# Kernel optimization log

Hardware: AMD Instinct MI355X
Metric: run time of the kernel (lower is better)

## Reference

```python
import jax, jax.numpy as jnp
import numpy as np

P_SCALAR = 40.0
NEG_INF = -1e30


def setup_inputs() -> dict:
    key = jax.random.key(0)
    k1, k2, k3, k4, k5 = jax.random.split(key, 5)
    B, Dk, Dv, T, H, W = 8, 128, 512, 2, 56, 56
    qkey = jax.random.normal(k1, (B, Dk, H, W), dtype=jnp.float32)
    qmask = jax.random.randint(k2, (B, 1, H, W), 0, 2).astype(jnp.bool_)
    mkey = jax.random.normal(k3, (B, Dk, T, H, W), dtype=jnp.float32)
    mval = jax.random.normal(k4, (B, Dv, T, H, W), dtype=jnp.float32)
    mmask = jax.random.randint(k5, (B, 1, T, H, W), 0, 2).astype(jnp.bool_)
    return {"qkey": qkey, "qmask": qmask, "mkey": mkey, "mval": mval, "mmask": mmask}


def reference(qkey, qmask, mkey, mval, mmask):
    # Faithful vectorized version of SegmentationAttentionSeparateModule.maskRead.
    # Torch loops over b, gathers masked query/memory columns, does
    # softmax(p_scalar * mk^T qk, dim=0) then mv @ p, scattering into zeros.
    # Equivalent dense math: masked softmax over memory positions, and zero
    # output at query positions outside qmask.
    B, Dk, H, W = qkey.shape
    Dv = mval.shape[1]
    M = H * W                       # query positions
    qk = qkey.reshape(B, Dk, M)     # [B, Dk, M]
    mk = mkey.reshape(B, Dk, -1)    # [B, Dk, N], N = T*H*W
    mv = mval.reshape(B, Dv, -1)    # [B, Dv, N]
    qm = qmask.reshape(B, 1, M)     # [B, 1, M]
    mm = mmask.reshape(B, -1)       # [B, N]

    # scores over memory (axis 1) per query column, p_scalar * mk^T qk
    scores = P_SCALAR * jnp.einsum('bdn,bdm->bnm', mk, qk)       # [B, N, M]
    scores = jnp.where(mm[:, :, None], scores, NEG_INF)
    p = jax.nn.softmax(scores, axis=1)                           # softmax over memory
    p = jnp.where(mm[:, :, None], p, 0.0)                        # guard all-masked rows
    qread = jnp.einsum('bdn,bnm->bdm', mv, p)                    # [B, Dv, M]
    qread = jnp.where(qm, qread, 0.0)                            # only masked query cols
    return qread.reshape(B, Dv, H, W)
```

## Files before the change

### kernel.cpp

```cpp
#include <hip/hip_runtime.h>
#include <stdint.h>

#define B_    8
#define DK_   128
#define DV_   512
#define M_    3136
#define N_    6272
#define MTILES_ 49
#define NSEG_ 8
#define TH_   30.0f
#define MARGIN_ 36.0f
#define BKT_  64

typedef short bf16x8 __attribute__((ext_vector_type(8)));
typedef float f32x16 __attribute__((ext_vector_type(16)));
typedef unsigned short u16x8 __attribute__((ext_vector_type(8)));

__device__ __forceinline__ unsigned fkey(float x) {
  unsigned u = __float_as_uint(x);
  return (u & 0x80000000u) ? ~u : (u | 0x80000000u);
}
__device__ __forceinline__ float fdec(unsigned k) {
  return __uint_as_float((k & 0x80000000u) ? (k & 0x7fffffffu) : ~k);
}
__device__ __forceinline__ unsigned short f2bf(float x) {
  unsigned u = __float_as_uint(x);
  return (unsigned short)((u + 0x7fffu + ((u >> 16) & 1u)) >> 16);
}
__device__ __forceinline__ unsigned pk2(float x, float y) {
  return (unsigned)f2bf(x) | ((unsigned)f2bf(y) << 16);
}
__device__ __forceinline__ float bf2f(unsigned short h) {
  return __uint_as_float(((unsigned)h) << 16);
}

__global__ __launch_bounds__(256)
void scan_masks(const int* __restrict__ qmask, const int* __restrict__ mmask,
                int* __restrict__ qlist, int* __restrict__ nlist,
                int* __restrict__ qcnt, int* __restrict__ ncnt) {
  int b = blockIdx.x;
  int tid = threadIdx.x, lane = tid & 63, wv = tid >> 6;
  __shared__ int wsum[4];
  __shared__ int cbase;
  if (tid == 0) cbase = 0;
  __syncthreads();
  for (int base = 0; base < M_; base += 256) {
    int i = base + tid;
    int flag = (i < M_) ? (qmask[b * M_ + i] != 0) : 0;
    unsigned long long bal = __ballot(flag);
    int prefix = __popcll(bal & ((1ull << lane) - 1ull));
    if (lane == 0) wsum[wv] = __popcll(bal);
    __syncthreads();
    int woff = 0;
    for (int t = 0; t < wv; ++t) woff += wsum[t];
    int total = wsum[0] + wsum[1] + wsum[2] + wsum[3];
    if (flag) qlist[b * M_ + cbase + woff + prefix] = i;
    __syncthreads();
    if (tid == 0) cbase += total;
    __syncthreads();
  }
  if (tid == 0) { qcnt[b] = cbase; cbase = 0; }
  __syncthreads();
  for (int base = 0; base < N_; base += 256) {
    int i = base + tid;
    int flag = (i < N_) ? (mmask[b * N_ + i] != 0) : 0;
    unsigned long long bal = __ballot(flag);
    int prefix = __popcll(bal & ((1ull << lane) - 1ull));
    if (lane == 0) wsum[wv] = __popcll(bal);
    __syncthreads();
    int woff = 0;
    for (int t = 0; t < wv; ++t) woff += wsum[t];
    int total = wsum[0] + wsum[1] + wsum[2] + wsum[3];
    if (flag) nlist[b * N_ + cbase + woff + prefix] = i;
    __syncthreads();
    if (tid == 0) cbase += total;
    __syncthreads();
  }
  if (tid == 0) ncnt[b] = cbase;
}

__global__ __launch_bounds__(256)
void transpose_key(const float* __restrict__ src, float* __restrict__ dst,
                   int X, float scale) {
  __shared__ float T[64][65];
  int b = blockIdx.z, dt = blockIdx.y, xt = blockIdx.x;
  int lane = threadIdx.x & 63, ri = threadIdx.x >> 6;
  #pragma unroll
  for (int k = 0; k < 16; ++k) {
    int dl = ri * 16 + k;
    T[dl][lane] = src[((size_t)b * DK_ + dt * 64 + dl) * X + xt * 64 + lane];
  }
  __syncthreads();
  #pragma unroll
  for (int k = 0; k < 16; ++k) {
    int xl = ri * 16 + k;
    dst[((size_t)b * X + xt * 64 + xl) * DK_ + dt * 64 + lane] = scale * T[lane][xl];
  }
}

__global__ __launch_bounds__(256)
void transpose_val(const float* __restrict__ mval, unsigned short* __restrict__ mvalT) {
  __shared__ float T[64][65];
  int b = blockIdx.z, dvt = blockIdx.y, nt = blockIdx.x;
  int lane = threadIdx.x & 63, ri = threadIdx.x >> 6;
  #pragma unroll
  for (int k = 0; k < 16; ++k) {
    int dvl = ri * 16 + k;
    T[dvl][lane] = mval[((size_t)b * DV_ + dvt * 64 + dvl) * N_ + nt * 64 + lane];
  }
  __syncthreads();
  #pragma unroll
  for (int k = 0; k < 16; ++k) {
    int nl = ri * 16 + k;
    mvalT[((size_t)b * N_ + nt * 64 + nl) * DV_ + dvt * 64 + lane] = f2bf(T[lane][nl]);
  }
}

__global__ __launch_bounds__(256, 4)
void score_mfma(const float* __restrict__ qkeyT, const float* __restrict__ mkeyT,
                const int* __restrict__ qlist, const int* __restrict__ nlist,
                const int* __restrict__ qcnt, const int* __restrict__ ncnt,
                unsigned* __restrict__ maxkey, unsigned* __restrict__ bcnt,
                unsigned* __restrict__ bucket) {
  int bid = blockIdx.x;
  int seg = bid & (NSEG_ - 1);
  int t   = bid >> 3;
  int mt  = t % MTILES_;
  int b   = t / MTILES_;
  int mc = qcnt[b];
  if (mt * 64 >= mc) return;
  int nc = ncnt[b];
  int ntiles = (nc + 63) >> 6;
  int t0 = (ntiles * seg) / NSEG_;
  int t1 = (ntiles * (seg + 1)) / NSEG_;
  if (t0 >= t1) return;

  __shared__ unsigned short Qs[64 * 128];
  __shared__ unsigned short Ks[64 * 128];
  __shared__ int Morig[64];
  __shared__ int Norig[64];
  __shared__ unsigned runkey[64];
  char* Qsb = (char*)Qs;
  char* Ksb = (char*)Ks;

  int tid = threadIdx.x;
  int lane = tid & 63, wv = tid >> 6;
  int wn = wv & 1, wm = wv >> 1;
  int l31 = lane & 31, lhi = lane >> 5;

  for (int i = tid; i < 2048; i += 256) {
    int row = i >> 5;
    int k4 = (i & 31) << 2;
    int cm = mt * 64 + row;
    int col = (cm < mc) ? qlist[b * M_ + cm] : qlist[b * M_];
    if (k4 == 0) Morig[row] = (cm < mc) ? col : -1;
    float4 v = *(const float4*)&qkeyT[((size_t)b * M_ + col) * DK_ + k4];
    uint2 w;
    w.x = pk2(v.x, v.y);
    w.y = pk2(v.z, v.w);
    *(uint2*)(Qsb + (row << 8) + (((unsigned)(k4 << 1)) ^ ((row & 7) << 4))) = w;
  }
  if (tid < 64) runkey[tid] = 0u;
  __syncthreads();

  int arow = wn * 32 + l31;
  int brow = wm * 32 + l31;
  int klo  = lhi << 4;
  int aswz = (arow & 7) << 4;
  int bswz = (brow & 7) << 4;

  for (int tt = t0; tt < t1; ++tt) {
    int nbase = tt << 6;
    for (int i = tid; i < 2048; i += 256) {
      int row = i >> 5;
      int k4 = (i & 31) << 2;
      int jn = nbase + row;
      int ncol = (jn < nc) ? nlist[b * N_ + jn] : nlist[b * N_];
      if (k4 == 0) Norig[row] = (jn < nc) ? ncol : -1;
      float4 v = *(const float4*)&mkeyT[((size_t)b * N_ + ncol) * DK_ + k4];
      uint2 w;
      w.x = pk2(v.x, v.y);
      w.y = pk2(v.z, v.w);
      *(uint2*)(Ksb + (row << 8) + (((unsigned)(k4 << 1)) ^ ((row & 7) << 4))) = w;
    }
    __syncthreads();

    f32x16 acc;
    #pragma unroll
    for (int r = 0; r < 16; ++r) acc[r] = 0.0f;
    #pragma unroll
    for (int kc = 0; kc < 8; ++kc) {
      int koff = (kc << 5) | klo;
      bf16x8 af = *(const bf16x8*)(Ksb + (arow << 8) + (koff ^ aswz));
      bf16x8 bq = *(const bf16x8*)(Qsb + (brow << 8) + (koff ^ bswz));
      acc = __builtin_amdgcn_mfma_f32_32x32x16_bf16(af, bq, acc, 0, 0, 0);
    }

    float cmx = acc[0];
    #pragma unroll
    for (int r = 1; r < 16; ++r) cmx = fmaxf(cmx, acc[r]);
    cmx = fmaxf(cmx, __shfl_xor(cmx, 32));
    if (lane < 32) atomicMax(&runkey[wm * 32 + l31], fkey(cmx));
    __syncthreads();
    if (tid < 64 && Morig[tid] >= 0) {
      unsigned mine = runkey[tid];
      unsigned old = atomicMax(&maxkey[b * M_ + Morig[tid]], mine);
      if (old > mine) runkey[tid] = old;
    }
    __syncthreads();
    {
      int mloc = wm * 32 + l31;
      int mo = Morig[mloc];
      if (mo >= 0) {
        float thr = fdec(runkey[mloc]) - MARGIN_;
        #pragma unroll
        for (int r = 0; r < 16; ++r) {
          if (acc[r] >= thr) {
            int nl = wn * 32 + (r & 3) + ((r >> 2) << 3) + (lhi << 2);
            int no = Norig[nl];
            if (no >= 0) {
              unsigned slot = atomicAdd(&bcnt[b * M_ + mo], 1u);
              if (slot < (unsigned)BKT_)
                bucket[(((size_t)(b * M_ + mo)) << 6) + slot] = (unsigned)no;
            }
          }
        }
      }
    }
    __syncthreads();
  }
}

__device__ __forceinline__ float dot128(const float* __restrict__ q,
                                        const float* __restrict__ k) {
  float s = 0.f;
  #pragma unroll 8
  for (int i = 0; i < DK_; i += 4) {
    float4 a = *(const float4*)&q[i];
    float4 bb = *(const float4*)&k[i];
    s += a.x * bb.x + a.y * bb.y + a.z * bb.z + a.w * bb.w;
  }
  return s;
}

__global__ __launch_bounds__(256)
void pv_exact(const float* __restrict__ qkeyT, const float* __restrict__ mkeyT,
              const unsigned short* __restrict__ mvalT,
              const int* __restrict__ qlist, const int* __restrict__ qcnt,
              const int* __restrict__ nlist, const int* __restrict__ ncnt,
              const unsigned* __restrict__ bcnt, const unsigned* __restrict__ bucket,
              float* __restrict__ outT) {
  int b = blockIdx.y;
  int wv = threadIdx.x >> 6, lane = threadIdx.x & 63;
  int c = blockIdx.x * 4 + wv;
  if (c >= qcnt[b]) return;
  int m = qlist[b * M_ + c];
  unsigned cnt = bcnt[b * M_ + m];
  const float* qrow = qkeyT + ((size_t)b * M_ + m) * DK_;
  float acc[8] = {0.f, 0.f, 0.f, 0.f, 0.f, 0.f, 0.f, 0.f};
  float lsum = 0.f;

  if (cnt <= (unsigned)BKT_) {
    int n = -1;
    if (lane < (int)cnt) n = (int)bucket[(((size_t)(b * M_ + m)) << 6) + lane];
    float sv = -3.0e38f;
    if (n >= 0) sv = dot128(qrow, mkeyT + ((size_t)b * N_ + n) * DK_);
    float mx = sv;
    #pragma unroll
    for (int o = 32; o > 0; o >>= 1) mx = fmaxf(mx, __shfl_xor(mx, o));
    float e = (n >= 0 && sv >= mx - TH_) ? expf(sv - mx) : 0.f;
    lsum = e;
    #pragma unroll
    for (int o = 32; o > 0; o >>= 1) lsum += __shfl_xor(lsum, o);
    unsigned long long alive = __ballot(e > 0.f);
    while (alive) {
      int lb = __ffsll((unsigned long long)alive) - 1;
      alive &= alive - 1;
      float w = __shfl(e, lb);
      int nn = __shfl(n, lb);
      u16x8 vvv = *(const u16x8*)(mvalT + ((size_t)b * N_ + nn) * DV_ + lane * 8);
      #pragma unroll
      for (int r = 0; r < 8; ++r) acc[r] += w * bf2f(vvv[r]);
    }
  } else {
    int nc = ncnt[b];
    float mx = -3.0e38f;
    for (int base = 0; base < nc; base += 64) {
      int jn = base + lane;
      float sv = -3.0e38f;
      if (jn < nc) {
        int n = nlist[b * N_ + jn];
        sv = dot128(qrow, mkeyT + ((size_t)b * N_ + n) * DK_);
      }
      mx = fmaxf(mx, sv);
    }
    #pragma unroll
    for (int o = 32; o > 0; o >>= 1) mx = fmaxf(mx, __shfl_xor(mx, o));
    for (int base = 0; base < nc; base += 64) {
      int jn = base + lane;
      int n = -1;
      float sv = -3.0e38f;
      if (jn < nc) {
        n = nlist[b * N_ + jn];
        sv = dot128(qrow, mkeyT + ((size_t)b * N_ + n) * DK_);
      }
      float e = (n >= 0 && sv >= mx - TH_) ? expf(sv - mx) : 0.f;
      lsum += e;
      unsigned long long alive = __ballot(e > 0.f);
      while (alive) {
        int lb = __ffsll((unsigned long long)alive) - 1;
        alive &= alive - 1;
        float w = __shfl(e, lb);
        int nn = __shfl(n, lb);
        u16x8 vvv = *(const u16x8*)(mvalT + ((size_t)b * N_ + nn) * DV_ + lane * 8);
        #pragma unroll
        for (int r = 0; r < 8; ++r) acc[r] += w * bf2f(vvv[r]);
      }
    }
    #pragma unroll
    for (int o = 32; o > 0; o >>= 1) lsum += __shfl_xor(lsum, o);
  }

  float inv = (lsum > 0.f) ? 1.0f / lsum : 0.0f;
  float* op = outT + ((size_t)b * M_ + m) * DV_ + lane * 8;
  float4 o0 = make_float4(acc[0] * inv, acc[1] * inv, acc[2] * inv, acc[3] * inv);
  float4 o1 = make_float4(acc[4] * inv, acc[5] * inv, acc[6] * inv, acc[7] * inv);
  *(float4*)&op[0] = o0;
  *(float4*)&op[4] = o1;
}

__global__ __launch_bounds__(256)
void finalize_T(const float* __restrict__ outT, const int* __restrict__ qmask,
                float* __restrict__ out) {
  __shared__ float T[64][65];
  int b = blockIdx.z, dvt = blockIdx.y, mt = blockIdx.x;
  int lane = threadIdx.x & 63, ri = threadIdx.x >> 6;
  #pragma unroll
  for (int k = 0; k < 16; ++k) {
    int ml = ri * 16 + k;
    int m = mt * 64 + ml;
    bool act = (qmask[b * M_ + m] != 0);
    T[ml][lane] = act ? outT[((size_t)b * M_ + m) * DV_ + dvt * 64 + lane] : 0.f;
  }
  __syncthreads();
  #pragma unroll
  for (int k = 0; k < 16; ++k) {
    int dvl = ri * 16 + k;
    out[((size_t)b * DV_ + dvt * 64 + dvl) * M_ + mt * 64 + lane] = T[lane][dvl];
  }
}

extern "C" void kernel_launch(void* const* d_in, const int* in_sizes, int n_in,
                              void* d_out, int out_size, void* d_ws, size_t ws_size,
                              hipStream_t stream) {
  const float* qkey  = (const float*)d_in[0];
  const int*   qmask = (const int*)d_in[1];
  const float* mkey  = (const float*)d_in[2];
  const float* mval  = (const float*)d_in[3];
  const int*   mmask = (const int*)d_in[4];
  float* out = (float*)d_out;

  uint8_t* w = (uint8_t*)d_ws;
  unsigned*       maxkey = (unsigned*)(w + 0);
  unsigned*       bcnt   = (unsigned*)(w + 100352);
  int*            qcnt   = (int*)(w + 200704);
  int*            ncnt   = (int*)(w + 200736);
  int*            qlist  = (int*)(w + 200832);
  int*            nlist  = (int*)(w + 301184);
  unsigned*       bucket = (unsigned*)(w + 501888);
  float*          qkeyT  = (float*)(w + 6924416);
  float*          mkeyT  = (float*)(w + 19769472);
  float*          outT   = (float*)(w + 45459584);
  unsigned short* mvalT  = (unsigned short*)(w + 96839808);

  hipMemsetAsync(d_ws, 0, 200832, stream);

  scan_masks<<<B_, 256, 0, stream>>>(qmask, mmask, qlist, nlist, qcnt, ncnt);
  transpose_key<<<dim3(M_ / 64, DK_ / 64, B_), 256, 0, stream>>>(qkey, qkeyT, M_, 40.0f);
  transpose_key<<<dim3(N_ / 64, DK_ / 64, B_), 256, 0, stream>>>(mkey, mkeyT, N_, 1.0f);
  transpose_val<<<dim3(N_ / 64, DV_ / 64, B_), 256, 0, stream>>>(mval, mvalT);

  score_mfma<<<B_ * MTILES_ * NSEG_, 256, 0, stream>>>(
      qkeyT, mkeyT, qlist, nlist, qcnt, ncnt, maxkey, bcnt, bucket);

  pv_exact<<<dim3((M_ + 3) / 4, B_), 256, 0, stream>>>(
      qkeyT, mkeyT, mvalT, qlist, qcnt, nlist, ncnt, bcnt, bucket, outT);

  finalize_T<<<dim3(M_ / 64, DV_ / 64, B_), 256, 0, stream>>>(outT, qmask, out);
}
```

Measured before the change: 229.6 us.

## Enlarge score tiles, precompute bf16 keys, bf16 output staging, parallel mask scans

The score kernel now covers 128 query rows per block, with each wave computing two 32x32 MFMA tiles that share one query fragment, and it loads bf16 keys prepared ahead of time by the transpose kernels. The per-tile float-to-bf16 packing is gone. Mask scans for query and memory run in separate blocks. The intermediate output is stored as bf16 rather than fp32, roughly halving its traffic but lowering its precision before finalize. The transposes now write both fp32 and bf16 copies, and the larger LDS footprint reduces occupancy.

```diff
diff --git a/kernel.cpp b/kernel.cpp
--- a/kernel.cpp
+++ b/kernel.cpp
@@ -6,7 +6,7 @@
 #define DV_   512
 #define M_    3136
 #define N_    6272
-#define MTILES_ 49
+#define MT128_ 25
 #define NSEG_ 8
 #define TH_   30.0f
 #define MARGIN_ 36.0f
@@ -26,9 +26,6 @@
 __device__ __forceinline__ unsigned short f2bf(float x) {
   unsigned u = __float_as_uint(x);
   return (unsigned short)((u + 0x7fffu + ((u >> 16) & 1u)) >> 16);
-}
-__device__ __forceinline__ unsigned pk2(float x, float y) {
-  return (unsigned)f2bf(x) | ((unsigned)f2bf(y) << 16);
 }
 __device__ __forceinline__ float bf2f(unsigned short h) {
   return __uint_as_float(((unsigned)h) << 16);
@@ -44,9 +41,12 @@
   __shared__ int cbase;
   if (tid == 0) cbase = 0;
   __syncthreads();
-  for (int base = 0; base < M_; base += 256) {
+  const int* src = (blockIdx.y == 0) ? (qmask + b * M_) : (mmask + b * N_);
+  int* dst = (blockIdx.y == 0) ? (qlist + b * M_) : (nlist + b * N_);
+  int len = (blockIdx.y == 0) ? M_ : N_;
+  for (int base = 0; base < len; base += 256) {
     int i = base + tid;
-    int flag = (i < M_) ? (qmask[b * M_ + i] != 0) : 0;
+    int flag = (i < len) ? (src[i] != 0) : 0;
     unsigned long long bal = __ballot(flag);
     int prefix = __popcll(bal & ((1ull << lane) - 1ull));
     if (lane == 0) wsum[wv] = __popcll(bal);
@@ -54,34 +54,19 @@
     int woff = 0;
     for (int t = 0; t < wv; ++t) woff += wsum[t];
     int total = wsum[0] + wsum[1] + wsum[2] + wsum[3];
-    if (flag) qlist[b * M_ + cbase + woff + prefix] = i;
+    if (flag) dst[cbase + woff + prefix] = i;
     __syncthreads();
     if (tid == 0) cbase += total;
     __syncthreads();
   }
-  if (tid == 0) { qcnt[b] = cbase; cbase = 0; }
-  __syncthreads();
-  for (int base = 0; base < N_; base += 256) {
-    int i = base + tid;
-    int flag = (i < N_) ? (mmask[b * N_ + i] != 0) : 0;
-    unsigned long long bal = __ballot(flag);
-    int prefix = __popcll(bal & ((1ull << lane) - 1ull));
-    if (lane == 0) wsum[wv] = __popcll(bal);
-    __syncthreads();
-    int woff = 0;
-    for (int t = 0; t < wv; ++t) woff += wsum[t];
-    int total = wsum[0] + wsum[1] + wsum[2] + wsum[3];
-    if (flag) nlist[b * N_ + cbase + woff + prefix] = i;
-    __syncthreads();
-    if (tid == 0) cbase += total;
-    __syncthreads();
-  }
-  if (tid == 0) ncnt[b] = cbase;
-}
-
-__global__ __launch_bounds__(256)
-void transpose_key(const float* __restrict__ src, float* __restrict__ dst,
-                   int X, float scale) {
+  if (tid == 0) {
+    if (blockIdx.y == 0) qcnt[b] = cbase; else ncnt[b] = cbase;
+  }
+}
+
+__global__ __launch_bounds__(256)
+void transpose_key(const float* __restrict__ src, float* __restrict__ dstf,
+                   unsigned short* __restrict__ dstb, int X, float scale) {
   __shared__ float T[64][65];
   int b = blockIdx.z, dt = blockIdx.y, xt = blockIdx.x;
   int lane = threadIdx.x & 63, ri = threadIdx.x >> 6;
@@ -94,7 +79,10 @@
   #pragma unroll
   for (int k = 0; k < 16; ++k) {
     int xl = ri * 16 + k;
-    dst[((size_t)b * X + xt * 64 + xl) * DK_ + dt * 64 + lane] = scale * T[lane][xl];
+    float v = scale * T[lane][xl];
+    size_t idx = ((size_t)b * X + xt * 64 + xl) * DK_ + dt * 64 + lane;
+    dstf[idx] = v;
+    dstb[idx] = f2bf(v);
   }
 }
 
@@ -116,8 +104,8 @@
   }
 }
 
-__global__ __launch_bounds__(256, 4)
-void score_mfma(const float* __restrict__ qkeyT, const float* __restrict__ mkeyT,
+__global__ __launch_bounds__(256, 3)
+void score_mfma(const unsigned short* __restrict__ qkb, const unsigned short* __restrict__ mkb,
                 const int* __restrict__ qlist, const int* __restrict__ nlist,
                 const int* __restrict__ qcnt, const int* __restrict__ ncnt,
                 unsigned* __restrict__ maxkey, unsigned* __restrict__ bcnt,
@@ -125,99 +113,102 @@
   int bid = blockIdx.x;
   int seg = bid & (NSEG_ - 1);
   int t   = bid >> 3;
-  int mt  = t % MTILES_;
-  int b   = t / MTILES_;
+  int mt  = t % MT128_;
+  int b   = t / MT128_;
   int mc = qcnt[b];
-  if (mt * 64 >= mc) return;
+  if (mt * 128 >= mc) return;
   int nc = ncnt[b];
   int ntiles = (nc + 63) >> 6;
   int t0 = (ntiles * seg) / NSEG_;
   int t1 = (ntiles * (seg + 1)) / NSEG_;
   if (t0 >= t1) return;
 
-  __shared__ unsigned short Qs[64 * 128];
+  __shared__ unsigned short Qs[128 * 128];
   __shared__ unsigned short Ks[64 * 128];
-  __shared__ int Morig[64];
-  __shared__ int Norig[64];
-  __shared__ unsigned runkey[64];
+  __shared__ int Morig[128];
+  __shared__ int NorigBuf[2][64];
+  __shared__ unsigned runkey[128];
   char* Qsb = (char*)Qs;
   char* Ksb = (char*)Ks;
 
   int tid = threadIdx.x;
   int lane = tid & 63, wv = tid >> 6;
-  int wn = wv & 1, wm = wv >> 1;
   int l31 = lane & 31, lhi = lane >> 5;
+  int mrow = wv * 32 + l31;
 
   for (int i = tid; i < 2048; i += 256) {
-    int row = i >> 5;
-    int k4 = (i & 31) << 2;
-    int cm = mt * 64 + row;
+    int row = i >> 4, ck = i & 15;
+    int cm = mt * 128 + row;
     int col = (cm < mc) ? qlist[b * M_ + cm] : qlist[b * M_];
-    if (k4 == 0) Morig[row] = (cm < mc) ? col : -1;
-    float4 v = *(const float4*)&qkeyT[((size_t)b * M_ + col) * DK_ + k4];
-    uint2 w;
-    w.x = pk2(v.x, v.y);
-    w.y = pk2(v.z, v.w);
-    *(uint2*)(Qsb + (row << 8) + (((unsigned)(k4 << 1)) ^ ((row & 7) << 4))) = w;
-  }
-  if (tid < 64) runkey[tid] = 0u;
-  __syncthreads();
-
-  int arow = wn * 32 + l31;
-  int brow = wm * 32 + l31;
-  int klo  = lhi << 4;
-  int aswz = (arow & 7) << 4;
-  int bswz = (brow & 7) << 4;
+    if (ck == 0) Morig[row] = (cm < mc) ? col : -1;
+    uint4 v = *(const uint4*)&qkb[((size_t)b * M_ + col) * DK_ + ck * 8];
+    *(uint4*)(Qsb + (row << 8) + ((ck ^ (row & 7)) << 4)) = v;
+  }
+  if (tid < 128) runkey[tid] = 0u;
+  __syncthreads();
+
+  int qswz = (mrow & 7) << 4;
+  int kswz = (l31 & 7) << 4;
 
   for (int tt = t0; tt < t1; ++tt) {
     int nbase = tt << 6;
-    for (int i = tid; i < 2048; i += 256) {
-      int row = i >> 5;
-      int k4 = (i & 31) << 2;
+    int par = tt & 1;
+    for (int i = tid; i < 1024; i += 256) {
+      int row = i >> 4, ck = i & 15;
       int jn = nbase + row;
       int ncol = (jn < nc) ? nlist[b * N_ + jn] : nlist[b * N_];
-      if (k4 == 0) Norig[row] = (jn < nc) ? ncol : -1;
-      float4 v = *(const float4*)&mkeyT[((size_t)b * N_ + ncol) * DK_ + k4];
-      uint2 w;
-      w.x = pk2(v.x, v.y);
-      w.y = pk2(v.z, v.w);
-      *(uint2*)(Ksb + (row << 8) + (((unsigned)(k4 << 1)) ^ ((row & 7) << 4))) = w;
-    }
-    __syncthreads();
-
-    f32x16 acc;
-    #pragma unroll
-    for (int r = 0; r < 16; ++r) acc[r] = 0.0f;
+      if (ck == 0) NorigBuf[par][row] = (jn < nc) ? ncol : -1;
+      uint4 v = *(const uint4*)&mkb[((size_t)b * N_ + ncol) * DK_ + ck * 8];
+      *(uint4*)(Ksb + (row << 8) + ((ck ^ (row & 7)) << 4)) = v;
+    }
+    __syncthreads();
+
+    f32x16 acc0, acc1;
+    #pragma unroll
+    for (int r = 0; r < 16; ++r) { acc0[r] = 0.0f; acc1[r] = 0.0f; }
     #pragma unroll
     for (int kc = 0; kc < 8; ++kc) {
-      int koff = (kc << 5) | klo;
-      bf16x8 af = *(const bf16x8*)(Ksb + (arow << 8) + (koff ^ aswz));
-      bf16x8 bq = *(const bf16x8*)(Qsb + (brow << 8) + (koff ^ bswz));
-      acc = __builtin_amdgcn_mfma_f32_32x32x16_bf16(af, bq, acc, 0, 0, 0);
-    }
-
-    float cmx = acc[0];
-    #pragma unroll
-    for (int r = 1; r < 16; ++r) cmx = fmaxf(cmx, acc[r]);
+      int koff = (kc << 5) | (lhi << 4);
+      bf16x8 bq = *(const bf16x8*)(Qsb + (mrow << 8) + (koff ^ qswz));
+      bf16x8 a0 = *(const bf16x8*)(Ksb + (l31 << 8) + (koff ^ kswz));
+      bf16x8 a1 = *(const bf16x8*)(Ksb + ((32 + l31) << 8) + (koff ^ kswz));
+      acc0 = __builtin_amdgcn_mfma_f32_32x32x16_bf16(a0, bq, acc0, 0, 0, 0);
+      acc1 = __builtin_amdgcn_mfma_f32_32x32x16_bf16(a1, bq, acc1, 0, 0, 0);
+    }
+
+    float cmx = fmaxf(acc0[0], acc1[0]);
+    #pragma unroll
+    for (int r = 1; r < 16; ++r) cmx = fmaxf(cmx, fmaxf(acc0[r], acc1[r]));
     cmx = fmaxf(cmx, __shfl_xor(cmx, 32));
-    if (lane < 32) atomicMax(&runkey[wm * 32 + l31], fkey(cmx));
-    __syncthreads();
-    if (tid < 64 && Morig[tid] >= 0) {
+    if (lane < 32) {
+      unsigned k = fkey(cmx);
+      if (k > runkey[mrow]) runkey[mrow] = k;
+    }
+    __syncthreads();
+    if (tid < 128 && Morig[tid] >= 0) {
       unsigned mine = runkey[tid];
       unsigned old = atomicMax(&maxkey[b * M_ + Morig[tid]], mine);
       if (old > mine) runkey[tid] = old;
     }
     __syncthreads();
     {
-      int mloc = wm * 32 + l31;
-      int mo = Morig[mloc];
+      int mo = Morig[mrow];
       if (mo >= 0) {
-        float thr = fdec(runkey[mloc]) - MARGIN_;
+        float thr = fdec(runkey[mrow]) - MARGIN_;
         #pragma unroll
         for (int r = 0; r < 16; ++r) {
-          if (acc[r] >= thr) {
-            int nl = wn * 32 + (r & 3) + ((r >> 2) << 3) + (lhi << 2);
-            int no = Norig[nl];
+          if (acc0[r] >= thr) {
+            int nl = (r & 3) + ((r >> 2) << 3) + (lhi << 2);
+            int no = NorigBuf[par][nl];
+            if (no >= 0) {
+              unsigned slot = atomicAdd(&bcnt[b * M_ + mo], 1u);
+              if (slot < (unsigned)BKT_)
+                bucket[(((size_t)(b * M_ + mo)) << 6) + slot] = (unsigned)no;
+            }
+          }
+          if (acc1[r] >= thr) {
+            int nl = 32 + (r & 3) + ((r >> 2) << 3) + (lhi << 2);
+            int no = NorigBuf[par][nl];
             if (no >= 0) {
               unsigned slot = atomicAdd(&bcnt[b * M_ + mo], 1u);
               if (slot < (unsigned)BKT_)
@@ -249,7 +240,7 @@
               const int* __restrict__ qlist, const int* __restrict__ qcnt,
               const int* __restrict__ nlist, const int* __restrict__ ncnt,
               const unsigned* __restrict__ bcnt, const unsigned* __restrict__ bucket,
-              float* __restrict__ outT) {
+              unsigned short* __restrict__ outT) {
   int b = blockIdx.y;
   int wv = threadIdx.x >> 6, lane = threadIdx.x & 63;
   int c = blockIdx.x * 4 + wv;
@@ -322,15 +313,14 @@
   }
 
   float inv = (lsum > 0.f) ? 1.0f / lsum : 0.0f;
-  float* op = outT + ((size_t)b * M_ + m) * DV_ + lane * 8;
-  float4 o0 = make_float4(acc[0] * inv, acc[1] * inv, acc[2] * inv, acc[3] * inv);
-  float4 o1 = make_float4(acc[4] * inv, acc[5] * inv, acc[6] * inv, acc[7] * inv);
-  *(float4*)&op[0] = o0;
-  *(float4*)&op[4] = o1;
-}
-
-__global__ __launch_bounds__(256)
-void finalize_T(const float* __restrict__ outT, const int* __restrict__ qmask,
+  u16x8 ov;
+  #pragma unroll
+  for (int r = 0; r < 8; ++r) ov[r] = f2bf(acc[r] * inv);
+  *(u16x8*)(outT + ((size_t)b * M_ + m) * DV_ + lane * 8) = ov;
+}
+
+__global__ __launch_bounds__(256)
+void finalize_T(const unsigned short* __restrict__ outT, const int* __restrict__ qmask,
                 float* __restrict__ out) {
   __shared__ float T[64][65];
   int b = blockIdx.z, dvt = blockIdx.y, mt = blockIdx.x;
@@ -340,7 +330,7 @@
     int ml = ri * 16 + k;
     int m = mt * 64 + ml;
     bool act = (qmask[b * M_ + m] != 0);
-    T[ml][lane] = act ? outT[((size_t)b * M_ + m) * DV_ + dvt * 64 + lane] : 0.f;
+    T[ml][lane] = act ? bf2f(outT[((size_t)b * M_ + m) * DV_ + dvt * 64 + lane]) : 0.f;
   }
   __syncthreads();
   #pragma unroll
@@ -370,21 +360,23 @@
   unsigned*       bucket = (unsigned*)(w + 501888);
   float*          qkeyT  = (float*)(w + 6924416);
   float*          mkeyT  = (float*)(w + 19769472);
-  float*          outT   = (float*)(w + 45459584);
-  unsigned short* mvalT  = (unsigned short*)(w + 96839808);
+  unsigned short* qkb    = (unsigned short*)(w + 45459584);
+  unsigned short* mkb    = (unsigned short*)(w + 51882112);
+  unsigned short* outTb  = (unsigned short*)(w + 64727168);
+  unsigned short* mvalT  = (unsigned short*)(w + 90417280);
 
   hipMemsetAsync(d_ws, 0, 200832, stream);
 
-  scan_masks<<<B_, 256, 0, stream>>>(qmask, mmask, qlist, nlist, qcnt, ncnt);
-  transpose_key<<<dim3(M_ / 64, DK_ / 64, B_), 256, 0, stream>>>(qkey, qkeyT, M_, 40.0f);
-  transpose_key<<<dim3(N_ / 64, DK_ / 64, B_), 256, 0, stream>>>(mkey, mkeyT, N_, 1.0f);
+  scan_masks<<<dim3(B_, 2), 256, 0, stream>>>(qmask, mmask, qlist, nlist, qcnt, ncnt);
+  transpose_key<<<dim3(M_ / 64, DK_ / 64, B_), 256, 0, stream>>>(qkey, qkeyT, qkb, M_, 40.0f);
+  transpose_key<<<dim3(N_ / 64, DK_ / 64, B_), 256, 0, stream>>>(mkey, mkeyT, mkb, N_, 1.0f);
   transpose_val<<<dim3(N_ / 64, DV_ / 64, B_), 256, 0, stream>>>(mval, mvalT);
 
-  score_mfma<<<B_ * MTILES_ * NSEG_, 256, 0, stream>>>(
-      qkeyT, mkeyT, qlist, nlist, qcnt, ncnt, maxkey, bcnt, bucket);
+  score_mfma<<<B_ * MT128_ * NSEG_, 256, 0, stream>>>(
+      qkb, mkb, qlist, nlist, qcnt, ncnt, maxkey, bcnt, bucket);
 
   pv_exact<<<dim3((M_ + 3) / 4, B_), 256, 0, stream>>>(
-      qkeyT, mkeyT, mvalT, qlist, qcnt, nlist, ncnt, bcnt, bucket, outT);
-
-  finalize_T<<<dim3(M_ / 64, DV_ / 64, B_), 256, 0, stream>>>(outT, qmask, out);
-}
+      qkeyT, mkeyT, mvalT, qlist, qcnt, nlist, ncnt, bcnt, bucket, outTb);
+
+  finalize_T<<<dim3(M_ / 64, DV_ / 64, B_), 256, 0, stream>>>(outTb, qmask, out);
+}
```

Measured after the change: 212.2 us. 1.08x faster.
